# Kernel tuning notes

Measured on AMD Instinct MI355X. Metric: run time of the kernel, lower is better.

## Reference

```python
import jax, jax.numpy as jnp
import numpy as np

B, L, D = 4096, 50, 64
NU, NI, NR = 100000, 100000, 5


def setup_inputs() -> dict:
    key = jax.random.key(0)
    ks = jax.random.split(key, 16)
    s = 0.02
    inp = {
        "nodes_v": jax.random.randint(ks[0], (B,), 0, NI),
        "neigh_u": jax.random.randint(ks[1], (B, L), 0, NU),
        "neigh_r": jax.random.randint(ks[2], (B, L), 0, NR),
        "embed_u": jax.random.normal(ks[3], (NU, D)) * s,
        "embed_i": jax.random.normal(ks[4], (NI, D)) * s,
        "embed_r": jax.random.normal(ks[5], (NR, D)) * s,
        # gv MLP: Linear(2D,D) ReLU Linear(D,D) ReLU Linear(D,D)
        "gv_w1": jax.random.normal(ks[6], (2 * D, D)) * s, "gv_b1": jnp.zeros((D,)),
        "gv_w2": jax.random.normal(ks[7], (D, D)) * s,     "gv_b2": jnp.zeros((D,)),
        "gv_w3": jax.random.normal(ks[8], (D, D)) * s,     "gv_b3": jnp.zeros((D,)),
        # attention MLP: Linear(2D,D) ReLU Linear(D,D) ReLU Linear(D,1), softmax over neighbors
        "att_w1": jax.random.normal(ks[9], (2 * D, D)) * s, "att_b1": jnp.zeros((D,)),
        "att_w2": jax.random.normal(ks[10], (D, D)) * s,    "att_b2": jnp.zeros((D,)),
        "att_w3": jax.random.normal(ks[11], (D, 1)) * s,    "att_b3": jnp.zeros((1,)),
        # combine: Linear(2D,D) ReLU Linear(D,D) ReLU
        "wr1_w": jax.random.normal(ks[12], (2 * D, D)) * s, "wr1_b": jnp.zeros((D,)),
        "wr2_w": jax.random.normal(ks[13], (D, D)) * s,     "wr2_b": jnp.zeros((D,)),
    }
    return inp


def reference(nodes_v, neigh_u, neigh_r, embed_u, embed_i, embed_r,
              gv_w1, gv_b1, gv_w2, gv_b2, gv_w3, gv_b3,
              att_w1, att_b1, att_w2, att_b2, att_w3, att_b3,
              wr1_w, wr1_b, wr2_w, wr2_b):
    qj = embed_i[nodes_v]            # [B, D] item reps
    pt = embed_u[neigh_u]            # [B, L, D] neighbor user reps
    er = embed_r[neigh_r]            # [B, L, D] rating reps
    # fusion MLP g(.)
    x = jnp.concatenate([pt, er], axis=-1)                    # [B, L, 2D]
    h = jax.nn.relu(x @ gv_w1 + gv_b1)
    h = jax.nn.relu(h @ gv_w2 + gv_b2)
    fjt = h @ gv_w3 + gv_b3                                   # [B, L, D]
    # attention over neighbors (dropout is identity in eval mode)
    q_rep = jnp.broadcast_to(qj[:, None, :], fjt.shape)       # [B, L, D]
    a = jnp.concatenate([fjt, q_rep], axis=-1)                # [B, L, 2D]
    a = jax.nn.relu(a @ att_w1 + att_b1)
    a = jax.nn.relu(a @ att_w2 + att_b2)
    scores = (a @ att_w3 + att_b3)[..., 0]                    # [B, L]
    mu = jax.nn.softmax(scores, axis=1)                       # softmax over neighbors
    zj = jnp.einsum("bld,bl->bd", fjt, mu)                   # weighted aggregation
    # combine aggregated neighborhood with item's own embedding (2D -> D)
    z = jax.nn.relu(jnp.concatenate([zj, qj], axis=-1) @ wr1_w + wr1_b)
    out = jax.nn.relu(z @ wr2_w + wr2_b)                      # [B, D]
    return out
```

## Files before the change

### kernel.cpp

```cpp
#include <hip/hip_runtime.h>

typedef __bf16 bf16;
typedef short s16x8 __attribute__((ext_vector_type(8)));
typedef __bf16 b16x8 __attribute__((ext_vector_type(8)));
typedef float f32x4 __attribute__((ext_vector_type(4)));

#define B_   4096
#define L_   50
#define SH   72

#define OFF_W1F  0
#define OFF_W2F  8192
#define OFF_W3F  12288
#define OFF_WCF  16384
#define OFF_A2F  20480
#define OFF_R1T  24576
#define OFF_R2T  32768
#define WT_TOTAL 36864
#define BIAS1P_BYTE 73728
#define CQ_BYTE     73984

#define PREP_W_BLOCKS 145
#define PREP_C_BLOCKS 1024

__device__ __forceinline__ unsigned short f2b(float f) {
    __bf16 h = (__bf16)f;
    return __builtin_bit_cast(unsigned short, h);
}
__device__ __forceinline__ unsigned pack2(float a, float b) {
    return (unsigned)f2b(a) | ((unsigned)f2b(b) << 16);
}
__device__ __forceinline__ s16x8 mkfrag(float4 a, float4 b) {
    union { s16x8 v; unsigned u[4]; } r;
    r.u[0] = pack2(a.x, a.y); r.u[1] = pack2(a.z, a.w);
    r.u[2] = pack2(b.x, b.y); r.u[3] = pack2(b.z, b.w);
    return r.v;
}
__device__ __forceinline__ f32x4 mfma16(s16x8 a, s16x8 b, f32x4 c) {
    return __builtin_amdgcn_mfma_f32_16x16x32_bf16(a, b, c, 0, 0, 0);
}

extern "C" __global__ void prep_all(const float* __restrict__ w1, const float* __restrict__ w2,
                                    const float* __restrict__ w3, const float* __restrict__ a1,
                                    const float* __restrict__ a2, const float* __restrict__ r1,
                                    const float* __restrict__ r2, const float* __restrict__ gb3,
                                    const float* __restrict__ ab1,
                                    const int* __restrict__ nodes_v, const float* __restrict__ embed_i,
                                    bf16* __restrict__ wt, float* __restrict__ bias1p,
                                    float* __restrict__ cq)
{
    if (blockIdx.x >= PREP_W_BLOCKS) {
        int gid = (blockIdx.x - PREP_W_BLOCKS) * 256 + threadIdx.x;
        int b = gid >> 6, n = gid & 63;
        int v = nodes_v[b];
        const float* q = embed_i + v * 64;
        float s0 = 0.f, s1 = 0.f, s2 = 0.f, s3 = 0.f;
#pragma unroll
        for (int k = 0; k < 64; k += 4) {
            s0 = fmaf(q[k],     a1[(64 + k) * 64 + n],     s0);
            s1 = fmaf(q[k + 1], a1[(64 + k + 1) * 64 + n], s1);
            s2 = fmaf(q[k + 2], a1[(64 + k + 2) * 64 + n], s2);
            s3 = fmaf(q[k + 3], a1[(64 + k + 3) * 64 + n], s3);
        }
        cq[gid] = (s0 + s1) + (s2 + s3);
        return;
    }
    int i = blockIdx.x * 256 + threadIdx.x;
    if (i >= WT_TOTAL + 64) return;
    if (i >= WT_TOTAL) {
        int n = i - WT_TOTAL;
        float s0 = ab1[n], s1 = 0.f, s2 = 0.f, s3 = 0.f;
#pragma unroll
        for (int t = 0; t < 64; t += 4) {
            s0 = fmaf(gb3[t],     a1[t * 64 + n],       s0);
            s1 = fmaf(gb3[t + 1], a1[(t + 1) * 64 + n], s1);
            s2 = fmaf(gb3[t + 2], a1[(t + 2) * 64 + n], s2);
            s3 = fmaf(gb3[t + 3], a1[(t + 3) * 64 + n], s3);
        }
        bias1p[n] = (s0 + s1) + (s2 + s3);
        return;
    }
    float val;
    if (i < OFF_R1T) {
        int off, kind;
        if      (i < OFF_W2F) { off = OFF_W1F; kind = 0; }
        else if (i < OFF_W3F) { off = OFF_W2F; kind = 1; }
        else if (i < OFF_WCF) { off = OFF_W3F; kind = 2; }
        else if (i < OFF_A2F) { off = OFF_WCF; kind = 3; }
        else                  { off = OFF_A2F; kind = 4; }
        int local = i - off;
        int f = local >> 9, lane = (local >> 3) & 63, j = local & 7;
        int kt = f >> 2, nt = f & 3, quad = lane >> 4, m = lane & 15;
        int k = kt * 32 + quad * 8 + j;
        int n = nt * 16 + m;
        if (kind == 0)      val = w1[k * 64 + n];
        else if (kind == 1) val = w2[k * 64 + n];
        else if (kind == 2) val = w3[k * 64 + n];
        else if (kind == 4) val = a2[k * 64 + n];
        else {
            float s0 = 0.f, s1 = 0.f, s2 = 0.f, s3 = 0.f;
#pragma unroll
            for (int t = 0; t < 64; t += 4) {
                float4 w = *(const float4*)(w3 + k * 64 + t);
                s0 = fmaf(w.x, a1[t * 64 + n],       s0);
                s1 = fmaf(w.y, a1[(t + 1) * 64 + n], s1);
                s2 = fmaf(w.z, a1[(t + 2) * 64 + n], s2);
                s3 = fmaf(w.w, a1[(t + 3) * 64 + n], s3);
            }
            val = (s0 + s1) + (s2 + s3);
        }
    }
    else if (i < OFF_R2T) { int li = i - OFF_R1T; int n = li >> 7, k = li & 127; val = r1[k * 64 + n]; }
    else                  { int li = i - OFF_R2T; int n = li >> 6, k = li & 63;  val = r2[k * 64 + n]; }
    wt[i] = (bf16)val;
}

extern "C" __global__ void __launch_bounds__(256, 2)
dense_fused(const int* __restrict__ nodes_v, const int* __restrict__ neigh_u,
            const int* __restrict__ neigh_r,
            const float* __restrict__ embed_u, const float* __restrict__ embed_i,
            const float* __restrict__ embed_r,
            const float* __restrict__ gv_b1, const float* __restrict__ gv_b2,
            const float* __restrict__ gv_b3,
            const float* __restrict__ att_b2, const float* __restrict__ att_w3,
            const float* __restrict__ wr1_b, const float* __restrict__ wr2_b,
            const bf16* __restrict__ wt, const float* __restrict__ cq,
            const float* __restrict__ bias1p, float* __restrict__ out)
{
    __shared__ __align__(16) bf16 H[64 * SH];
    __shared__ float csS[64];
    __shared__ float qsh[64];
    __shared__ float scs[64];
    __shared__ float zp[4 * 64];

    const int tid = threadIdx.x;
    const int lane = tid & 63, wave = tid >> 6;
    const int m = lane & 15, quad = lane >> 4;
    const int b = blockIdx.x;

    if (tid < 64)        csS[tid] = cq[b * 64 + tid] + bias1p[tid];
    else if (tid < 128)  qsh[tid - 64] = embed_i[nodes_v[b] * 64 + (tid - 64)];

    const int l = min(wave * 16 + m, L_ - 1);
    const int u = neigh_u[b * L_ + l];
    const int r = neigh_r[b * L_ + l];

    bf16* Hw = H + wave * 16 * SH;

    {
        const float* pu = embed_u + u * 64;
        const float* pr = embed_r + r * 64;
        f32x4 ac[4] = {};
#pragma unroll
        for (int kt = 0; kt < 4; ++kt) {
            const float* sp = (kt < 2 ? pu : pr) + (kt & 1) * 32 + quad * 8;
            float4 aa = *(const float4*)sp, ab = *(const float4*)(sp + 4);
            s16x8 af = mkfrag(aa, ab);
#pragma unroll
            for (int nt = 0; nt < 4; ++nt) {
                s16x8 bw = *(const s16x8*)(wt + OFF_W1F + (kt * 4 + nt) * 512 + lane * 8);
                ac[nt] = mfma16(af, bw, ac[nt]);
            }
        }
#pragma unroll
        for (int nt = 0; nt < 4; ++nt) {
            int c = nt * 16 + m;
            float bv = gv_b1[c];
#pragma unroll
            for (int r4 = 0; r4 < 4; ++r4)
                Hw[(quad * 4 + r4) * SH + c] = (bf16)fmaxf(ac[nt][r4] + bv, 0.f);
        }
    }

    {
        f32x4 ac[4] = {};
#pragma unroll
        for (int kt = 0; kt < 2; ++kt) {
            s16x8 a = *(const s16x8*)(Hw + m * SH + kt * 32 + quad * 8);
#pragma unroll
            for (int nt = 0; nt < 4; ++nt) {
                s16x8 bw = *(const s16x8*)(wt + OFF_W2F + (kt * 4 + nt) * 512 + lane * 8);
                ac[nt] = mfma16(a, bw, ac[nt]);
            }
        }
#pragma unroll
        for (int nt = 0; nt < 4; ++nt) {
            int c = nt * 16 + m;
            float bv = gv_b2[c];
#pragma unroll
            for (int r4 = 0; r4 < 4; ++r4)
                Hw[(quad * 4 + r4) * SH + c] = (bf16)fmaxf(ac[nt][r4] + bv, 0.f);
        }
    }

    __syncthreads();

    f32x4 aF[4] = {};
    {
        f32x4 aA[4] = {};
#pragma unroll
        for (int kt = 0; kt < 2; ++kt) {
            s16x8 a = *(const s16x8*)(Hw + m * SH + kt * 32 + quad * 8);
#pragma unroll
            for (int nt = 0; nt < 4; ++nt) {
                s16x8 bF = *(const s16x8*)(wt + OFF_W3F + (kt * 4 + nt) * 512 + lane * 8);
                s16x8 bA = *(const s16x8*)(wt + OFF_WCF + (kt * 4 + nt) * 512 + lane * 8);
                aF[nt] = mfma16(a, bF, aF[nt]);
                aA[nt] = mfma16(a, bA, aA[nt]);
            }
        }
#pragma unroll
        for (int nt = 0; nt < 4; ++nt) {
            int c = nt * 16 + m;
            float b1v = csS[c];
#pragma unroll
            for (int r4 = 0; r4 < 4; ++r4)
                Hw[(quad * 4 + r4) * SH + c] = (bf16)fmaxf(aA[nt][r4] + b1v, 0.f);
        }
    }

    {
        f32x4 ac[4] = {};
#pragma unroll
        for (int kt = 0; kt < 2; ++kt) {
            s16x8 a = *(const s16x8*)(Hw + m * SH + kt * 32 + quad * 8);
#pragma unroll
            for (int nt = 0; nt < 4; ++nt) {
                s16x8 bw = *(const s16x8*)(wt + OFF_A2F + (kt * 4 + nt) * 512 + lane * 8);
                ac[nt] = mfma16(a, bw, ac[nt]);
            }
        }
        float sc[4] = {0.f, 0.f, 0.f, 0.f};
#pragma unroll
        for (int nt = 0; nt < 4; ++nt) {
            int c = nt * 16 + m;
            float b2v = att_b2[c], w3v = att_w3[c];
#pragma unroll
            for (int r4 = 0; r4 < 4; ++r4)
                sc[r4] += fmaxf(ac[nt][r4] + b2v, 0.f) * w3v;
        }
#pragma unroll
        for (int mask = 1; mask < 16; mask <<= 1)
#pragma unroll
            for (int r4 = 0; r4 < 4; ++r4) sc[r4] += __shfl_xor(sc[r4], mask);
        if (m == 0) {
#pragma unroll
            for (int r4 = 0; r4 < 4; ++r4)
                scs[wave * 16 + quad * 4 + r4] = sc[r4];
        }
    }
    __syncthreads();

    {
        float s = (lane < L_) ? scs[lane] : -1e30f;
        float mx = s;
#pragma unroll
        for (int off = 32; off; off >>= 1) mx = fmaxf(mx, __shfl_xor(mx, off));
        float e = (lane < L_) ? __expf(s - mx) : 0.f;
        float sum = e;
#pragma unroll
        for (int off = 32; off; off >>= 1) sum += __shfl_xor(sum, off);
        float mu = e / sum;

        float z[4] = {0.f, 0.f, 0.f, 0.f};
#pragma unroll
        for (int r4 = 0; r4 < 4; ++r4) {
            float mr = __shfl(mu, wave * 16 + quad * 4 + r4);
#pragma unroll
            for (int nt = 0; nt < 4; ++nt) z[nt] += aF[nt][r4] * mr;
        }
#pragma unroll
        for (int nt = 0; nt < 4; ++nt) {
            z[nt] += __shfl_xor(z[nt], 16);
            z[nt] += __shfl_xor(z[nt], 32);
        }
        if (quad == 0) {
#pragma unroll
            for (int nt = 0; nt < 4; ++nt) zp[wave * 64 + nt * 16 + m] = z[nt];
        }
    }
    __syncthreads();

    if (wave == 0) {
        const int d = lane;
        float z = zp[d] + zp[64 + d] + zp[128 + d] + zp[192 + d] + gv_b3[d];
        scs[d] = z;

        float accz = wr1_b[d];
        const bf16* r1 = wt + OFF_R1T + d * 128;
#pragma unroll
        for (int k8 = 0; k8 < 8; ++k8) {
            b16x8 wv = *(const b16x8*)(r1 + k8 * 8);
#pragma unroll
            for (int j = 0; j < 8; ++j) accz = fmaf((float)wv[j], scs[k8 * 8 + j], accz);
        }
#pragma unroll
        for (int k8 = 0; k8 < 8; ++k8) {
            b16x8 wv = *(const b16x8*)(r1 + 64 + k8 * 8);
#pragma unroll
            for (int j = 0; j < 8; ++j) accz = fmaf((float)wv[j], qsh[k8 * 8 + j], accz);
        }
        zp[d] = fmaxf(accz, 0.f);

        float acco = wr2_b[d];
        const bf16* r2 = wt + OFF_R2T + d * 64;
#pragma unroll
        for (int k8 = 0; k8 < 8; ++k8) {
            b16x8 wv = *(const b16x8*)(r2 + k8 * 8);
#pragma unroll
            for (int j = 0; j < 8; ++j) acco = fmaf((float)wv[j], zp[k8 * 8 + j], acco);
        }
        out[b * 64 + d] = fmaxf(acco, 0.f);
    }
}

extern "C" void kernel_launch(void* const* d_in, const int* in_sizes, int n_in,
                              void* d_out, int out_size, void* d_ws, size_t ws_size,
                              hipStream_t stream)
{
    const int* nodes_v = (const int*)d_in[0];
    const int* neigh_u = (const int*)d_in[1];
    const int* neigh_r = (const int*)d_in[2];
    const float* embed_u = (const float*)d_in[3];
    const float* embed_i = (const float*)d_in[4];
    const float* embed_r = (const float*)d_in[5];
    const float* gv_w1  = (const float*)d_in[6];  const float* gv_b1 = (const float*)d_in[7];
    const float* gv_w2  = (const float*)d_in[8];  const float* gv_b2 = (const float*)d_in[9];
    const float* gv_w3  = (const float*)d_in[10]; const float* gv_b3 = (const float*)d_in[11];
    const float* att_w1 = (const float*)d_in[12]; const float* att_b1 = (const float*)d_in[13];
    const float* att_w2 = (const float*)d_in[14]; const float* att_b2 = (const float*)d_in[15];
    const float* att_w3 = (const float*)d_in[16]; const float* att_b3 = (const float*)d_in[17];
    const float* wr1_w  = (const float*)d_in[18]; const float* wr1_b = (const float*)d_in[19];
    const float* wr2_w  = (const float*)d_in[20]; const float* wr2_b = (const float*)d_in[21];
    (void)att_b3;

    bf16*  wt     = (bf16*)d_ws;
    float* bias1p = (float*)((char*)d_ws + BIAS1P_BYTE);
    float* cq     = (float*)((char*)d_ws + CQ_BYTE);

    prep_all<<<PREP_W_BLOCKS + PREP_C_BLOCKS, 256, 0, stream>>>(
        gv_w1, gv_w2, gv_w3, att_w1, att_w2, wr1_w, wr2_w, gv_b3, att_b1,
        nodes_v, embed_i, wt, bias1p, cq);
    dense_fused<<<B_, 256, 0, stream>>>(nodes_v, neigh_u, neigh_r,
                                        embed_u, embed_i, embed_r,
                                        gv_b1, gv_b2, gv_b3, att_b2, att_w3,
                                        wr1_b, wr2_b, wt, cq, bias1p, (float*)d_out);
}
```

Baseline: 174.9 us.

## Process two items per block and stage MLP weights in shared memory

Each block now handles two batch items with 512 threads (eight waves) instead of one item with 256 threads. The bf16 weights for gv_w2, gv_w3, the fused attention layer-1 slice and att_w2 are copied once per block into a 32 KB LDS buffer. Their MFMA B-fragments are then read from LDS rather than from global memory. This is meant to cut repeated global/L2 weight traffic and amortise the weight load across twice as many neighbor rows. The cost is a per-block 32 KB copy, an extra barrier before layer 2, and much higher LDS use, which may limit how many blocks fit on a CU.

```diff
diff --git a/kernel.cpp b/kernel.cpp
--- a/kernel.cpp
+++ b/kernel.cpp
@@ -115,7 +115,7 @@
     wt[i] = (bf16)val;
 }
 
-extern "C" __global__ void __launch_bounds__(256, 2)
+extern "C" __global__ void __launch_bounds__(512, 2)
 dense_fused(const int* __restrict__ nodes_v, const int* __restrict__ neigh_u,
             const int* __restrict__ neigh_r,
             const float* __restrict__ embed_u, const float* __restrict__ embed_i,
@@ -127,25 +127,38 @@
             const bf16* __restrict__ wt, const float* __restrict__ cq,
             const float* __restrict__ bias1p, float* __restrict__ out)
 {
-    __shared__ __align__(16) bf16 H[64 * SH];
-    __shared__ float csS[64];
-    __shared__ float qsh[64];
-    __shared__ float scs[64];
-    __shared__ float zp[4 * 64];
+    __shared__ __align__(16) bf16 Ws[16384];
+    __shared__ __align__(16) bf16 H[128 * SH];
+    __shared__ float csS[128];
+    __shared__ float qsh[128];
+    __shared__ float scs[128];
+    float* zp = (float*)H;
 
     const int tid = threadIdx.x;
     const int lane = tid & 63, wave = tid >> 6;
     const int m = lane & 15, quad = lane >> 4;
-    const int b = blockIdx.x;
-
-    if (tid < 64)        csS[tid] = cq[b * 64 + tid] + bias1p[tid];
-    else if (tid < 128)  qsh[tid - 64] = embed_i[nodes_v[b] * 64 + (tid - 64)];
-
-    const int l = min(wave * 16 + m, L_ - 1);
-    const int u = neigh_u[b * L_ + l];
-    const int r = neigh_r[b * L_ + l];
-
-    bf16* Hw = H + wave * 16 * SH;
+    const int b0 = blockIdx.x * 2;
+    const int item_w = wave >> 2;
+    const int lbase = (wave & 3) * 16;
+
+    {
+        const uint4* src = (const uint4*)(wt + OFF_W2F);
+        uint4* dst = (uint4*)Ws;
+#pragma unroll
+        for (int it = 0; it < 4; ++it) dst[tid + it * 512] = src[tid + it * 512];
+    }
+    if (tid < 128) {
+        int item = tid >> 6, n = tid & 63;
+        csS[tid] = cq[(b0 + item) * 64 + n] + bias1p[n];
+        qsh[tid] = embed_i[nodes_v[b0 + item] * 64 + n];
+    }
+
+    const int bw = b0 + item_w;
+    const int l = min(lbase + m, L_ - 1);
+    const int u = neigh_u[bw * L_ + l];
+    const int r = neigh_r[bw * L_ + l];
+
+    bf16* Hw = H + (item_w * 64 + lbase) * SH;
 
     {
         const float* pu = embed_u + u * 64;
@@ -158,8 +171,8 @@
             s16x8 af = mkfrag(aa, ab);
 #pragma unroll
             for (int nt = 0; nt < 4; ++nt) {
-                s16x8 bw = *(const s16x8*)(wt + OFF_W1F + (kt * 4 + nt) * 512 + lane * 8);
-                ac[nt] = mfma16(af, bw, ac[nt]);
+                s16x8 bw_ = *(const s16x8*)(wt + OFF_W1F + (kt * 4 + nt) * 512 + lane * 8);
+                ac[nt] = mfma16(af, bw_, ac[nt]);
             }
         }
 #pragma unroll
@@ -172,6 +185,8 @@
         }
     }
 
+    __syncthreads();
+
     {
         f32x4 ac[4] = {};
 #pragma unroll
@@ -179,8 +194,8 @@
             s16x8 a = *(const s16x8*)(Hw + m * SH + kt * 32 + quad * 8);
 #pragma unroll
             for (int nt = 0; nt < 4; ++nt) {
-                s16x8 bw = *(const s16x8*)(wt + OFF_W2F + (kt * 4 + nt) * 512 + lane * 8);
-                ac[nt] = mfma16(a, bw, ac[nt]);
+                s16x8 b = *(const s16x8*)(Ws + (kt * 4 + nt) * 512 + lane * 8);
+                ac[nt] = mfma16(a, b, ac[nt]);
             }
         }
 #pragma unroll
@@ -193,8 +208,6 @@
         }
     }
 
-    __syncthreads();
-
     f32x4 aF[4] = {};
     {
         f32x4 aA[4] = {};
@@ -203,8 +216,8 @@
             s16x8 a = *(const s16x8*)(Hw + m * SH + kt * 32 + quad * 8);
 #pragma unroll
             for (int nt = 0; nt < 4; ++nt) {
-                s16x8 bF = *(const s16x8*)(wt + OFF_W3F + (kt * 4 + nt) * 512 + lane * 8);
-                s16x8 bA = *(const s16x8*)(wt + OFF_WCF + (kt * 4 + nt) * 512 + lane * 8);
+                s16x8 bF = *(const s16x8*)(Ws + 4096 + (kt * 4 + nt) * 512 + lane * 8);
+                s16x8 bA = *(const s16x8*)(Ws + 8192 + (kt * 4 + nt) * 512 + lane * 8);
                 aF[nt] = mfma16(a, bF, aF[nt]);
                 aA[nt] = mfma16(a, bA, aA[nt]);
             }
@@ -212,7 +225,7 @@
 #pragma unroll
         for (int nt = 0; nt < 4; ++nt) {
             int c = nt * 16 + m;
-            float b1v = csS[c];
+            float b1v = csS[item_w * 64 + c];
 #pragma unroll
             for (int r4 = 0; r4 < 4; ++r4)
                 Hw[(quad * 4 + r4) * SH + c] = (bf16)fmaxf(aA[nt][r4] + b1v, 0.f);
@@ -226,8 +239,8 @@
             s16x8 a = *(const s16x8*)(Hw + m * SH + kt * 32 + quad * 8);
 #pragma unroll
             for (int nt = 0; nt < 4; ++nt) {
-                s16x8 bw = *(const s16x8*)(wt + OFF_A2F + (kt * 4 + nt) * 512 + lane * 8);
-                ac[nt] = mfma16(a, bw, ac[nt]);
+                s16x8 b = *(const s16x8*)(Ws + 12288 + (kt * 4 + nt) * 512 + lane * 8);
+                ac[nt] = mfma16(a, b, ac[nt]);
             }
         }
         float sc[4] = {0.f, 0.f, 0.f, 0.f};
@@ -246,13 +259,13 @@
         if (m == 0) {
 #pragma unroll
             for (int r4 = 0; r4 < 4; ++r4)
-                scs[wave * 16 + quad * 4 + r4] = sc[r4];
+                scs[item_w * 64 + lbase + quad * 4 + r4] = sc[r4];
         }
     }
     __syncthreads();
 
     {
-        float s = (lane < L_) ? scs[lane] : -1e30f;
+        float s = (lane < L_) ? scs[item_w * 64 + lane] : -1e30f;
         float mx = s;
 #pragma unroll
         for (int off = 32; off; off >>= 1) mx = fmaxf(mx, __shfl_xor(mx, off));
@@ -265,7 +278,7 @@
         float z[4] = {0.f, 0.f, 0.f, 0.f};
 #pragma unroll
         for (int r4 = 0; r4 < 4; ++r4) {
-            float mr = __shfl(mu, wave * 16 + quad * 4 + r4);
+            float mr = __shfl(mu, lbase + quad * 4 + r4);
 #pragma unroll
             for (int nt = 0; nt < 4; ++nt) z[nt] += aF[nt][r4] * mr;
         }
@@ -281,10 +294,13 @@
     }
     __syncthreads();
 
-    if (wave == 0) {
+    if ((wave & 3) == 0) {
+        const int item = wave >> 2;
         const int d = lane;
-        float z = zp[d] + zp[64 + d] + zp[128 + d] + zp[192 + d] + gv_b3[d];
-        scs[d] = z;
+        float z = zp[(wave + 0) * 64 + d] + zp[(wave + 1) * 64 + d]
+                + zp[(wave + 2) * 64 + d] + zp[(wave + 3) * 64 + d] + gv_b3[d];
+        float* zsh = scs + item * 64;
+        zsh[d] = z;
 
         float accz = wr1_b[d];
         const bf16* r1 = wt + OFF_R1T + d * 128;
@@ -292,15 +308,16 @@
         for (int k8 = 0; k8 < 8; ++k8) {
             b16x8 wv = *(const b16x8*)(r1 + k8 * 8);
 #pragma unroll
-            for (int j = 0; j < 8; ++j) accz = fmaf((float)wv[j], scs[k8 * 8 + j], accz);
+            for (int j = 0; j < 8; ++j) accz = fmaf((float)wv[j], zsh[k8 * 8 + j], accz);
         }
 #pragma unroll
         for (int k8 = 0; k8 < 8; ++k8) {
             b16x8 wv = *(const b16x8*)(r1 + 64 + k8 * 8);
 #pragma unroll
-            for (int j = 0; j < 8; ++j) accz = fmaf((float)wv[j], qsh[k8 * 8 + j], accz);
-        }
-        zp[d] = fmaxf(accz, 0.f);
+            for (int j = 0; j < 8; ++j) accz = fmaf((float)wv[j], qsh[item * 64 + k8 * 8 + j], accz);
+        }
+        float* z2sh = zp + wave * 64;
+        z2sh[d] = fmaxf(accz, 0.f);
 
         float acco = wr2_b[d];
         const bf16* r2 = wt + OFF_R2T + d * 64;
@@ -308,9 +325,9 @@
         for (int k8 = 0; k8 < 8; ++k8) {
             b16x8 wv = *(const b16x8*)(r2 + k8 * 8);
 #pragma unroll
-            for (int j = 0; j < 8; ++j) acco = fmaf((float)wv[j], zp[k8 * 8 + j], acco);
-        }
-        out[b * 64 + d] = fmaxf(acco, 0.f);
+            for (int j = 0; j < 8; ++j) acco = fmaf((float)wv[j], z2sh[k8 * 8 + j], acco);
+        }
+        out[(b0 + item) * 64 + d] = fmaxf(acco, 0.f);
     }
 }
 
@@ -341,8 +358,8 @@
     prep_all<<<PREP_W_BLOCKS + PREP_C_BLOCKS, 256, 0, stream>>>(
         gv_w1, gv_w2, gv_w3, att_w1, att_w2, wr1_w, wr2_w, gv_b3, att_b1,
         nodes_v, embed_i, wt, bias1p, cq);
-    dense_fused<<<B_, 256, 0, stream>>>(nodes_v, neigh_u, neigh_r,
-                                        embed_u, embed_i, embed_r,
-                                        gv_b1, gv_b2, gv_b3, att_b2, att_w3,
-                                        wr1_b, wr2_b, wt, cq, bias1p, (float*)d_out);
-}
+    dense_fused<<<B_ / 2, 512, 0, stream>>>(nodes_v, neigh_u, neigh_r,
+                                            embed_u, embed_i, embed_r,
+                                            gv_b1, gv_b2, gv_b3, att_b2, att_w3,
+                                            wr1_b, wr2_b, wt, cq, bias1p, (float*)d_out);
+}
```

Result: faster. 168.3 us (-3.7%).
